# Kernel optimization log

Hardware: AMD Instinct MI355X
Metric: run time of the kernel (lower is better)

The kernel has to match this reference:

```python
import jax, jax.numpy as jnp
import numpy as np

HEADS = 4
NEG_SLOPE_ATT = 0.2   # GATConv default negative_slope
NEG_SLOPE_ACT = 0.01  # torch.nn.LeakyReLU default


def setup_inputs() -> dict:
    key = jax.random.key(0)
    ks = jax.random.split(key, 10)
    N, F_IN, C, NCLS, B = 100000, 128, 32, 10, 128
    E = 1600000
    x = jax.random.normal(ks[0], (N, F_IN), dtype=jnp.float32)
    edge_index = jax.random.randint(ks[1], (2, E), 0, N, dtype=jnp.int64)
    batch = jnp.sort(jax.random.randint(ks[2], (N,), 0, B, dtype=jnp.int64))
    # GATConv parameters (eval mode: dropout inactive)
    W = jax.random.normal(ks[3], (F_IN, HEADS * C), dtype=jnp.float32) / np.sqrt(F_IN)
    att_src = jax.random.normal(ks[4], (HEADS, C), dtype=jnp.float32) / np.sqrt(C)
    att_dst = jax.random.normal(ks[5], (HEADS, C), dtype=jnp.float32) / np.sqrt(C)
    bias = jnp.zeros((HEADS * C,), dtype=jnp.float32)
    lin_w = jax.random.normal(ks[6], (NCLS, HEADS * C), dtype=jnp.float32) / np.sqrt(HEADS * C)
    lin_b = jnp.zeros((NCLS,), dtype=jnp.float32)
    return {"x": x, "edge_index": edge_index, "batch": batch, "batch_size": B,
            "W": W, "att_src": att_src, "att_dst": att_dst, "bias": bias,
            "lin_w": lin_w, "lin_b": lin_b}


def _leaky(v, s):
    return jnp.where(v >= 0, v, s * v)


def reference(x, edge_index, batch, batch_size, W, att_src, att_dst, bias, lin_w, lin_b):
    N = x.shape[0]
    H, C = att_src.shape
    xh = (x @ W).reshape(N, H, C)                      # [N,H,C]
    # add self-loops (GATConv default add_self_loops=True)
    loops = jnp.arange(N, dtype=edge_index.dtype)
    src = jnp.concatenate([edge_index[0], loops])      # [E+N]
    dst = jnp.concatenate([edge_index[1], loops])
    a_src = jnp.einsum('nhc,hc->nh', xh, att_src)      # [N,H]
    a_dst = jnp.einsum('nhc,hc->nh', xh, att_dst)
    e = _leaky(a_src[src] + a_dst[dst], NEG_SLOPE_ATT) # [E+N,H]
    # segment softmax over incoming edges of each dst node
    m = jax.ops.segment_max(e, dst, num_segments=N)
    e = jnp.exp(e - m[dst])
    s = jax.ops.segment_sum(e, dst, num_segments=N)
    alpha = e / (s[dst] + 1e-16)                       # [E+N,H]
    msg = xh[src] * alpha[..., None]                   # [E+N,H,C]
    out = jax.ops.segment_sum(msg, dst, num_segments=N).reshape(N, H * C) + bias
    out = _leaky(out, NEG_SLOPE_ACT)
    # global mean pool per graph
    summed = jax.ops.segment_sum(out, batch, num_segments=batch_size)
    counts = jax.ops.segment_sum(jnp.ones((N,), dtype=out.dtype), batch, num_segments=batch_size)
    pooled = summed / jnp.maximum(counts, 1.0)[:, None]
    return pooled @ lin_w.T + lin_b
```

## Files before the change

kernel.cpp:

```cpp
#include <hip/hip_runtime.h>
#include <hip/hip_fp16.h>

#define HC 128
#define FIN 128
#define NHEAD 4
#define NS_ATT 0.2f
#define NS_ACT 0.01f
#define NBLK_P 256
#define BCAP 14336

typedef _Float16 half8 __attribute__((ext_vector_type(8)));
typedef float f32x4 __attribute__((ext_vector_type(4)));

__device__ __forceinline__ float lrelu(float v, float s) { return v >= 0.f ? v : s * v; }

__device__ __forceinline__ int lowerb(const int* __restrict__ a, int n, int v) {
  int lo = 0, hi = n;
  while (lo < hi) {
    int m = (lo + hi) >> 1;
    if (a[m] < v) lo = m + 1; else hi = m;
  }
  return lo;
}

__global__ __launch_bounds__(256) void k_hw(
    const int* __restrict__ ei, int* __restrict__ hist, int E, int NBUCK, int CH,
    const float* __restrict__ W, const float* __restrict__ att_s,
    const float* __restrict__ att_d, _Float16* __restrict__ Wh) {
  if (blockIdx.x >= NBLK_P) {
    const int nt = blockIdx.x - NBLK_P, t = threadIdx.x;
    const int kt = t >> 6, l = t & 63;
    const int c = nt * 16 + (l & 15);
    const int kbase = kt * 32 + (l >> 4) * 8;
    half8 v8;
#pragma unroll
    for (int j = 0; j < 8; ++j) {
      const int k = kbase + j;
      float v = 0.f;
      if (c < 128) {
        v = W[k * HC + c];
      } else if (c < 132) {
        const int h = c - 128;
        for (int cc = 0; cc < 32; ++cc) v += W[k * HC + h * 32 + cc] * att_s[h * 32 + cc];
      } else if (c < 136) {
        const int h = c - 132;
        for (int cc = 0; cc < 32; ++cc) v += W[k * HC + h * 32 + cc] * att_d[h * 32 + cc];
      }
      v8[j] = (_Float16)v;
    }
    ((half8*)Wh)[(nt * 4 + kt) * 64 + l] = v8;
    return;
  }
  __shared__ int lc[512];
  for (int i = threadIdx.x; i < NBUCK; i += 256) lc[i] = 0;
  __syncthreads();
  const int e0 = blockIdx.x * CH, e1 = min(E, e0 + CH);
  for (int e = e0 + threadIdx.x; e < e1; e += 256) {
    atomicAdd(&lc[ei[E + e] >> 9], 1);
  }
  __syncthreads();
  for (int i = threadIdx.x; i < NBUCK; i += 256) hist[i * NBLK_P + blockIdx.x] = lc[i];
}

__global__ __launch_bounds__(256) void k_xw(
    const float* __restrict__ x, const _Float16* __restrict__ Wh,
    _Float16* __restrict__ xh, float* __restrict__ a_src, float* __restrict__ a_dst,
    int N) {
  __shared__ _Float16 xs[4][16][HC + 8];
  const int wv = threadIdx.x >> 6, l = threadIdx.x & 63;
  const int r0 = blockIdx.x * 64 + wv * 16;
  if (r0 >= N) return;
  const int row_a = r0 + (l & 15);
  const long arow = (long)min(row_a, N - 1) * FIN;
  const int kg = (l >> 4) * 8;
  half8 afr[4];
#pragma unroll
  for (int kt = 0; kt < 4; ++kt) {
    const float4 p0 = *(const float4*)(x + arow + kt * 32 + kg);
    const float4 p1 = *(const float4*)(x + arow + kt * 32 + kg + 4);
    afr[kt][0] = (_Float16)p0.x; afr[kt][1] = (_Float16)p0.y;
    afr[kt][2] = (_Float16)p0.z; afr[kt][3] = (_Float16)p0.w;
    afr[kt][4] = (_Float16)p1.x; afr[kt][5] = (_Float16)p1.y;
    afr[kt][6] = (_Float16)p1.z; afr[kt][7] = (_Float16)p1.w;
  }
  const half8* __restrict__ Wh8 = (const half8*)Wh;
  const int rloc = (l >> 4) * 4;
  const int cc = l & 15;
#pragma unroll
  for (int nt = 0; nt < 9; ++nt) {
    half8 b0 = Wh8[(nt * 4 + 0) * 64 + l];
    half8 b1 = Wh8[(nt * 4 + 1) * 64 + l];
    half8 b2 = Wh8[(nt * 4 + 2) * 64 + l];
    half8 b3 = Wh8[(nt * 4 + 3) * 64 + l];
    f32x4 acc = {0.f, 0.f, 0.f, 0.f};
    acc = __builtin_amdgcn_mfma_f32_16x16x32_f16(afr[0], b0, acc, 0, 0, 0);
    acc = __builtin_amdgcn_mfma_f32_16x16x32_f16(afr[1], b1, acc, 0, 0, 0);
    acc = __builtin_amdgcn_mfma_f32_16x16x32_f16(afr[2], b2, acc, 0, 0, 0);
    acc = __builtin_amdgcn_mfma_f32_16x16x32_f16(afr[3], b3, acc, 0, 0, 0);
    if (nt < 8) {
      const int col = nt * 16 + cc;
#pragma unroll
      for (int r = 0; r < 4; ++r) xs[wv][rloc + r][col] = (_Float16)acc[r];
    } else if (cc < 8) {
      float* __restrict__ dst = (cc < 4) ? a_src : a_dst;
      const int h = cc & 3;
#pragma unroll
      for (int r = 0; r < 4; ++r) {
        const int row = r0 + rloc + r;
        if (row < N) dst[row * NHEAD + h] = acc[r];
      }
    }
  }
#pragma unroll
  for (int i = 0; i < 4; ++i) {
    const int lr = (l >> 4) + i * 4;
    const int row = r0 + lr;
    if (row < N) {
      const uint4 v = *(const uint4*)&xs[wv][lr][(l & 15) * 8];
      *(uint4*)(xh + (long)row * HC + (l & 15) * 8) = v;
    }
  }
}

__global__ void k_scanA(const int* __restrict__ cnt, int* __restrict__ offs,
                        int* __restrict__ part, int N) {
  __shared__ int s[256];
  int t = threadIdx.x, i = blockIdx.x * 256 + t;
  int v = (i < N) ? cnt[i] : 0;
  s[t] = v;
#pragma unroll
  for (int off = 1; off < 256; off <<= 1) {
    __syncthreads();
    int u = (t >= off) ? s[t - off] : 0;
    __syncthreads();
    s[t] += u;
  }
  if (i < N) offs[i] = s[t] - v;
  if (t == 255) part[blockIdx.x] = s[255];
}

__global__ void k_scanB(int* __restrict__ part, int NB) {
  __shared__ int s[1024];
  int t = threadIdx.x;
  int v = (t < NB) ? part[t] : 0;
  s[t] = v;
#pragma unroll
  for (int off = 1; off < 1024; off <<= 1) {
    __syncthreads();
    int u = (t >= off) ? s[t - off] : 0;
    __syncthreads();
    s[t] += u;
  }
  if (t < NB) part[t] = s[t] - v;
  if (t == 1023) part[NB] = s[1023];
}

__global__ void k_scanC(int* __restrict__ offs, const int* __restrict__ part, int N, int NB) {
  int i = blockIdx.x * 256 + threadIdx.x;
  if (i < N) offs[i] += part[i >> 8];
  else if (i == N) offs[N] = part[NB];
}

__global__ __launch_bounds__(256) void k_part(const int* __restrict__ ei,
                                              const int* __restrict__ histoffs,
                                              unsigned* __restrict__ ebuf,
                                              int E, int NBUCK, int CH) {
  __shared__ int lcur[512];
  for (int i = threadIdx.x; i < NBUCK; i += 256)
    lcur[i] = histoffs[i * NBLK_P + blockIdx.x];
  __syncthreads();
  const int e0 = blockIdx.x * CH, e1 = min(E, e0 + CH);
  for (int e = e0 + threadIdx.x; e < e1; e += 256) {
    const int s = ei[e], d = ei[E + e];
    const int pos = atomicAdd(&lcur[d >> 9], 1);
    ebuf[pos] = ((unsigned)(d & 511) << 18) | (unsigned)s;
  }
}

__global__ __launch_bounds__(256) void k_build(
    const int* __restrict__ histoffs, const unsigned* __restrict__ ebuf,
    int* __restrict__ csr_src, int* __restrict__ offs, int N) {
  const int b = blockIdx.x, t = threadIdx.x;
  const int n0 = b << 9, n1 = min(N, n0 + 512), nn = n1 - n0;
  const int eb0 = histoffs[b * NBLK_P];
  const int eb1 = histoffs[(b + 1) * NBLK_P];
  const int base = eb0 + n0;
  const int L = (eb1 - eb0) + nn;
  __shared__ int cnt2[512];
  __shared__ int scn[256];
  __shared__ int cur[512];
  __shared__ int lcsr[BCAP];
  cnt2[t] = 0; cnt2[t + 256] = 0;
  __syncthreads();
  for (int e = eb0 + t; e < eb1; e += 256) atomicAdd(&cnt2[ebuf[e] >> 18], 1);
  __syncthreads();
  const int i0 = 2 * t, i1 = 2 * t + 1;
  const int a0 = (i0 < nn) ? cnt2[i0] + 1 : 0;
  const int a1 = (i1 < nn) ? cnt2[i1] + 1 : 0;
  scn[t] = a0 + a1;
  for (int off = 1; off < 256; off <<= 1) {
    __syncthreads();
    int u = (t >= off) ? scn[t - off] : 0;
    __syncthreads();
    scn[t] += u;
  }
  __syncthreads();
  const int ex = scn[t] - (a0 + a1);
  const int o0 = ex, o1 = ex + a0;
  if (i0 < nn) offs[n0 + i0] = base + o0;
  if (i1 < nn) offs[n0 + i1] = base + o1;
  if (t == 255 && n1 == N) offs[N] = base + scn[255];
  if (L <= BCAP) {
    if (i0 < nn) { lcsr[o0] = n0 + i0; cur[i0] = o0 + 1; }
    if (i1 < nn) { lcsr[o1] = n0 + i1; cur[i1] = o1 + 1; }
    __syncthreads();
    for (int e = eb0 + t; e < eb1; e += 256) {
      const unsigned pk = ebuf[e];
      const int pos = atomicAdd(&cur[pk >> 18], 1);
      lcsr[pos] = (int)(pk & 0x3FFFFu);
    }
    __syncthreads();
    for (int i = t; i < L; i += 256) csr_src[base + i] = lcsr[i];
  } else {
    if (i0 < nn) { csr_src[base + o0] = n0 + i0; cur[i0] = base + o0 + 1; }
    if (i1 < nn) { csr_src[base + o1] = n0 + i1; cur[i1] = base + o1 + 1; }
    __syncthreads();
    for (int e = eb0 + t; e < eb1; e += 256) {
      const unsigned pk = ebuf[e];
      const int pos = atomicAdd(&cur[pk >> 18], 1);
      csr_src[pos] = (int)(pk & 0x3FFFFu);
    }
  }
}

__global__ __launch_bounds__(256) void k_agg(
    const int* __restrict__ csr_src, const int* __restrict__ offs,
    const float* __restrict__ a_src, const float* __restrict__ a_dst,
    const __half* __restrict__ xh, const float* __restrict__ bias,
    __half* __restrict__ xout, int N) {
  __shared__ float wls[4][64 * 5];
  __shared__ int sls[4][64];
  const int wv = threadIdx.x >> 6;
  const int wid = (blockIdx.x * 256 + threadIdx.x) >> 6;
  const int lane = threadIdx.x & 63;
  if (wid >= N) return;
  float* __restrict__ wl = wls[wv];
  int* __restrict__ sl = sls[wv];
  const int n = wid;
  const int o0 = offs[n], deg = offs[n + 1] - o0;
  const float4 dv = ((const float4*)a_dst)[n];
  const int l16 = lane & 15, g = lane >> 4, h = l16 >> 2;
  const uint4* __restrict__ xh16 = (const uint4*)xh;

  float4 sm = make_float4(0.f, 0.f, 0.f, 0.f);
  float acc[8] = {0.f, 0.f, 0.f, 0.f, 0.f, 0.f, 0.f, 0.f};

  for (int c0 = 0; c0 < deg; c0 += 64) {
    const int cl = min(64, deg - c0);
    if (lane < cl) {
      const int sj = csr_src[o0 + c0 + lane];
      const float4 av = ((const float4*)a_src)[sj];
      const float w0 = __expf(lrelu(av.x + dv.x, NS_ATT));
      const float w1 = __expf(lrelu(av.y + dv.y, NS_ATT));
      const float w2 = __expf(lrelu(av.z + dv.z, NS_ATT));
      const float w3 = __expf(lrelu(av.w + dv.w, NS_ATT));
      sm.x += w0; sm.y += w1; sm.z += w2; sm.w += w3;
      sl[lane] = sj;
      wl[lane * 5 + 0] = w0; wl[lane * 5 + 1] = w1;
      wl[lane * 5 + 2] = w2; wl[lane * 5 + 3] = w3;
    }
    for (int j = 0; j < cl; j += 16) {
      int s[4];
      float wsel[4];
      uint4 u[4];
#pragma unroll
      for (int q = 0; q < 4; ++q) {
        const int ee = j + q * 4 + g;
        const bool valid = ee < cl;
        const float wv_ = wl[ee * 5 + h];
        const int ss = sl[ee];
        wsel[q] = valid ? wv_ : 0.f;
        s[q] = valid ? ss : 0;
      }
#pragma unroll
      for (int q = 0; q < 4; ++q) {
        u[q] = xh16[(long)s[q] * 16 + l16];
      }
#pragma unroll
      for (int q = 0; q < 4; ++q) {
        const __half2* hp = (const __half2*)&u[q];
        const float2 f0 = __half22float2(hp[0]);
        const float2 f1 = __half22float2(hp[1]);
        const float2 f2 = __half22float2(hp[2]);
        const float2 f3 = __half22float2(hp[3]);
        acc[0] = fmaf(wsel[q], f0.x, acc[0]); acc[1] = fmaf(wsel[q], f0.y, acc[1]);
        acc[2] = fmaf(wsel[q], f1.x, acc[2]); acc[3] = fmaf(wsel[q], f1.y, acc[3]);
        acc[4] = fmaf(wsel[q], f2.x, acc[4]); acc[5] = fmaf(wsel[q], f2.y, acc[5]);
        acc[6] = fmaf(wsel[q], f3.x, acc[6]); acc[7] = fmaf(wsel[q], f3.y, acc[7]);
      }
    }
  }

#pragma unroll
  for (int m = 32; m >= 1; m >>= 1) {
    sm.x += __shfl_xor(sm.x, m);
    sm.y += __shfl_xor(sm.y, m);
    sm.z += __shfl_xor(sm.z, m);
    sm.w += __shfl_xor(sm.w, m);
  }
#pragma unroll
  for (int m = 32; m >= 16; m >>= 1) {
#pragma unroll
    for (int i = 0; i < 8; ++i) acc[i] += __shfl_xor(acc[i], m);
  }

  const float sh = (h == 0) ? sm.x : (h == 1) ? sm.y : (h == 2) ? sm.z : sm.w;
  const float inv = 1.f / (sh + 1e-16f);
  const int ch = l16 * 8 + g * 2;
  float r0 = lrelu(acc[2 * g] * inv + bias[ch], NS_ACT);
  float r1 = lrelu(acc[2 * g + 1] * inv + bias[ch + 1], NS_ACT);
  ((__half2*)(xout + (long)n * HC))[ch >> 1] = __floats2half2_rn(r0, r1);
}

__global__ __launch_bounds__(512) void k_poolfinal(
    const __half* __restrict__ xout, const int* __restrict__ batch,
    const float* __restrict__ lin_w, const float* __restrict__ lin_b,
    float* __restrict__ out, int N, int B) {
  const int b = blockIdx.x, t = threadIdx.x;
  const int lo = lowerb(batch, N, b);
  const int hi = lowerb(batch, N, b + 1);
  const int cnt = hi - lo;
  const int c2 = t & 63;
  const int rs = t >> 6;
  const __half2* __restrict__ xo2 = (const __half2*)xout;
  float ax = 0.f, ay = 0.f, bx2 = 0.f, by2 = 0.f;
  int r = lo + rs;
  for (; r + 8 < hi; r += 16) {
    float2 f0 = __half22float2(xo2[(long)r * 64 + c2]);
    float2 f1 = __half22float2(xo2[(long)(r + 8) * 64 + c2]);
    ax += f0.x; ay += f0.y; bx2 += f1.x; by2 += f1.y;
  }
  for (; r < hi; r += 8) {
    float2 f0 = __half22float2(xo2[(long)r * 64 + c2]);
    ax += f0.x; ay += f0.y;
  }
  __shared__ float2 sp[512];
  __shared__ float pl[HC];
  sp[t] = make_float2(ax + bx2, ay + by2);
  __syncthreads();
  if (t < 64) {
    float vx = 0.f, vy = 0.f;
#pragma unroll
    for (int i = 0; i < 8; ++i) {
      vx += sp[t + i * 64].x;
      vy += sp[t + i * 64].y;
    }
    const float c = fmaxf((float)cnt, 1.0f);
    pl[2 * t] = vx / c;
    pl[2 * t + 1] = vy / c;
  }
  __syncthreads();
  if (t < 10) {
    float a = lin_b[t];
    for (int k = 0; k < HC; ++k) a = fmaf(pl[k], lin_w[t * HC + k], a);
    out[b * 10 + t] = a;
  }
}

extern "C" void kernel_launch(void* const* d_in, const int* in_sizes, int n_in,
                              void* d_out, int out_size, void* d_ws, size_t ws_size,
                              hipStream_t stream) {
  const float* x = (const float*)d_in[0];
  const int* ei = (const int*)d_in[1];
  const int* batch = (const int*)d_in[2];
  const float* Wm = (const float*)d_in[4];
  const float* att_s = (const float*)d_in[5];
  const float* att_d = (const float*)d_in[6];
  const float* bias = (const float*)d_in[7];
  const float* lin_w = (const float*)d_in[8];
  const float* lin_b = (const float*)d_in[9];
  float* out = (float*)d_out;

  const int N = in_sizes[2];
  const int E = in_sizes[1] / 2;
  const int B = out_size / 10;
  const int NBUCK = (N + 511) >> 9;
  const int M = NBUCK * NBLK_P;
  const int NB2 = (M + 255) / 256;
  const int CH = (E + NBLK_P - 1) / NBLK_P;

  char* p = (char*)d_ws;
  auto carve = [&](size_t bytes) {
    void* r = (void*)p;
    p += (bytes + 255) & ~(size_t)255;
    return r;
  };
  __half* xh = (__half*)carve((size_t)N * HC * 2);
  __half* xout = (__half*)carve((size_t)N * HC * 2);
  float* a_src = (float*)carve((size_t)N * NHEAD * 4);
  float* a_dst = (float*)carve((size_t)N * NHEAD * 4);
  int* offs = (int*)carve((size_t)(N + 1) * 4);
  int* csr_src = (int*)carve((size_t)(N + (size_t)E) * 4);
  _Float16* Wh = (_Float16*)carve((size_t)9 * 4 * 64 * 8 * 2);

  char* q = (char*)xout;
  auto carve2 = [&](size_t bytes) {
    void* r = (void*)q;
    q += (bytes + 255) & ~(size_t)255;
    return r;
  };
  unsigned* ebuf = (unsigned*)carve2((size_t)E * 4);
  int* hist = (int*)carve2((size_t)M * 4);
  int* histoffs = (int*)carve2((size_t)(M + 1) * 4);
  int* part2 = (int*)carve2((size_t)(NB2 + 2) * 4);

  k_hw<<<NBLK_P + 9, 256, 0, stream>>>(ei, hist, E, NBUCK, CH, Wm, att_s, att_d, Wh);
  k_xw<<<(N + 63) / 64, 256, 0, stream>>>(x, Wh, (_Float16*)xh, a_src, a_dst, N);
  k_scanA<<<NB2, 256, 0, stream>>>(hist, histoffs, part2, M);
  k_scanB<<<1, 1024, 0, stream>>>(part2, NB2);
  k_scanC<<<(M + 256) / 256, 256, 0, stream>>>(histoffs, part2, M, NB2);
  k_part<<<NBLK_P, 256, 0, stream>>>(ei, histoffs, ebuf, E, NBUCK, CH);
  k_build<<<NBUCK, 256, 0, stream>>>(histoffs, ebuf, csr_src, offs, N);
  k_agg<<<(N + 3) / 4, 256, 0, stream>>>(csr_src, offs, a_src, a_dst, xh, bias, xout, N);
  k_poolfinal<<<B, 512, 0, stream>>>(xout, batch, lin_w, lin_b, out, N, B);
}
```

Baseline: 179.5 us.

## Fold histogram scan into partition kernel and merge histogram with XW GEMM

Removes the three separate scan kernels by having each partition block redundantly sum per-bucket counts across all 256 histogram blocks and scan the bucket totals itself. The edge histogram now runs as extra blocks of the x@W kernel instead of sharing a launch with weight prep, which gets its own small kernel. The aim is fewer kernel launches and serial dependencies. In exchange, every partition block does redundant global reads of the histogram, and the xs padding is enlarged.

```diff
diff --git a/kernel.cpp b/kernel.cpp
--- a/kernel.cpp
+++ b/kernel.cpp
@@ -23,50 +23,50 @@
   return lo;
 }
 
-__global__ __launch_bounds__(256) void k_hw(
-    const int* __restrict__ ei, int* __restrict__ hist, int E, int NBUCK, int CH,
-    const float* __restrict__ W, const float* __restrict__ att_s,
-    const float* __restrict__ att_d, _Float16* __restrict__ Wh) {
-  if (blockIdx.x >= NBLK_P) {
-    const int nt = blockIdx.x - NBLK_P, t = threadIdx.x;
-    const int kt = t >> 6, l = t & 63;
-    const int c = nt * 16 + (l & 15);
-    const int kbase = kt * 32 + (l >> 4) * 8;
-    half8 v8;
-#pragma unroll
-    for (int j = 0; j < 8; ++j) {
-      const int k = kbase + j;
-      float v = 0.f;
-      if (c < 128) {
-        v = W[k * HC + c];
-      } else if (c < 132) {
-        const int h = c - 128;
-        for (int cc = 0; cc < 32; ++cc) v += W[k * HC + h * 32 + cc] * att_s[h * 32 + cc];
-      } else if (c < 136) {
-        const int h = c - 132;
-        for (int cc = 0; cc < 32; ++cc) v += W[k * HC + h * 32 + cc] * att_d[h * 32 + cc];
-      }
-      v8[j] = (_Float16)v;
-    }
-    ((half8*)Wh)[(nt * 4 + kt) * 64 + l] = v8;
-    return;
-  }
-  __shared__ int lc[512];
-  for (int i = threadIdx.x; i < NBUCK; i += 256) lc[i] = 0;
-  __syncthreads();
-  const int e0 = blockIdx.x * CH, e1 = min(E, e0 + CH);
-  for (int e = e0 + threadIdx.x; e < e1; e += 256) {
-    atomicAdd(&lc[ei[E + e] >> 9], 1);
-  }
-  __syncthreads();
-  for (int i = threadIdx.x; i < NBUCK; i += 256) hist[i * NBLK_P + blockIdx.x] = lc[i];
-}
-
-__global__ __launch_bounds__(256) void k_xw(
+__global__ void k_wprep(const float* __restrict__ W, const float* __restrict__ att_s,
+                        const float* __restrict__ att_d, _Float16* __restrict__ Wh) {
+  const int nt = blockIdx.x, t = threadIdx.x;
+  const int kt = t >> 6, l = t & 63;
+  const int c = nt * 16 + (l & 15);
+  const int kbase = kt * 32 + (l >> 4) * 8;
+  half8 v8;
+#pragma unroll
+  for (int j = 0; j < 8; ++j) {
+    const int k = kbase + j;
+    float v = 0.f;
+    if (c < 128) {
+      v = W[k * HC + c];
+    } else if (c < 132) {
+      const int h = c - 128;
+      for (int cc = 0; cc < 32; ++cc) v += W[k * HC + h * 32 + cc] * att_s[h * 32 + cc];
+    } else if (c < 136) {
+      const int h = c - 132;
+      for (int cc = 0; cc < 32; ++cc) v += W[k * HC + h * 32 + cc] * att_d[h * 32 + cc];
+    }
+    v8[j] = (_Float16)v;
+  }
+  ((half8*)Wh)[(nt * 4 + kt) * 64 + l] = v8;
+}
+
+__global__ __launch_bounds__(256) void k_xwh(
     const float* __restrict__ x, const _Float16* __restrict__ Wh,
     _Float16* __restrict__ xh, float* __restrict__ a_src, float* __restrict__ a_dst,
-    int N) {
-  __shared__ _Float16 xs[4][16][HC + 8];
+    int N, int NXW,
+    const int* __restrict__ ei, int* __restrict__ hist, int E, int NBUCK, int CH) {
+  __shared__ _Float16 xs[4][16][HC + 16];
+  __shared__ int lc[512];
+  if (blockIdx.x >= NXW) {
+    const int b = blockIdx.x - NXW;
+    for (int i = threadIdx.x; i < NBUCK; i += 256) lc[i] = 0;
+    __syncthreads();
+    const int e0 = b * CH, e1 = min(E, e0 + CH);
+    for (int e = e0 + threadIdx.x; e < e1; e += 256) {
+      atomicAdd(&lc[ei[E + e] >> 9], 1);
+    }
+    __syncthreads();
+    for (int i = threadIdx.x; i < NBUCK; i += 256) hist[b * NBUCK + i] = lc[i];
+    return;
+  }
   const int wv = threadIdx.x >> 6, l = threadIdx.x & 63;
   const int r0 = blockIdx.x * 64 + wv * 16;
   if (r0 >= N) return;
@@ -122,55 +122,48 @@
   }
 }
 
-__global__ void k_scanA(const int* __restrict__ cnt, int* __restrict__ offs,
-                        int* __restrict__ part, int N) {
-  __shared__ int s[256];
-  int t = threadIdx.x, i = blockIdx.x * 256 + t;
-  int v = (i < N) ? cnt[i] : 0;
-  s[t] = v;
-#pragma unroll
-  for (int off = 1; off < 256; off <<= 1) {
-    __syncthreads();
-    int u = (t >= off) ? s[t - off] : 0;
-    __syncthreads();
-    s[t] += u;
-  }
-  if (i < N) offs[i] = s[t] - v;
-  if (t == 255) part[blockIdx.x] = s[255];
-}
-
-__global__ void k_scanB(int* __restrict__ part, int NB) {
-  __shared__ int s[1024];
-  int t = threadIdx.x;
-  int v = (t < NB) ? part[t] : 0;
-  s[t] = v;
-#pragma unroll
-  for (int off = 1; off < 1024; off <<= 1) {
-    __syncthreads();
-    int u = (t >= off) ? s[t - off] : 0;
-    __syncthreads();
-    s[t] += u;
-  }
-  if (t < NB) part[t] = s[t] - v;
-  if (t == 1023) part[NB] = s[1023];
-}
-
-__global__ void k_scanC(int* __restrict__ offs, const int* __restrict__ part, int N, int NB) {
-  int i = blockIdx.x * 256 + threadIdx.x;
-  if (i < N) offs[i] += part[i >> 8];
-  else if (i == N) offs[N] = part[NB];
-}
-
 __global__ __launch_bounds__(256) void k_part(const int* __restrict__ ei,
-                                              const int* __restrict__ histoffs,
+                                              const int* __restrict__ hist,
+                                              int* __restrict__ histbase,
                                               unsigned* __restrict__ ebuf,
                                               int E, int NBUCK, int CH) {
   __shared__ int lcur[512];
-  for (int i = threadIdx.x; i < NBUCK; i += 256)
-    lcur[i] = histoffs[i * NBLK_P + blockIdx.x];
-  __syncthreads();
-  const int e0 = blockIdx.x * CH, e1 = min(E, e0 + CH);
-  for (int e = e0 + threadIdx.x; e < e1; e += 256) {
+  __shared__ int tot[512];
+  __shared__ int scn[256];
+  const int b = blockIdx.x, t = threadIdx.x;
+  for (int i = t; i < NBUCK; i += 256) {
+    int sum = 0, pre = 0;
+    for (int bb = 0; bb < NBLK_P; ++bb) {
+      const int v = hist[bb * NBUCK + i];
+      sum += v;
+      if (bb < b) pre += v;
+    }
+    tot[i] = sum;
+    lcur[i] = pre;
+  }
+  __syncthreads();
+  const int i0 = 2 * t, i1 = 2 * t + 1;
+  const int a0 = (i0 < NBUCK) ? tot[i0] : 0;
+  const int a1 = (i1 < NBUCK) ? tot[i1] : 0;
+  scn[t] = a0 + a1;
+  for (int off = 1; off < 256; off <<= 1) {
+    __syncthreads();
+    int u = (t >= off) ? scn[t - off] : 0;
+    __syncthreads();
+    scn[t] += u;
+  }
+  __syncthreads();
+  const int ex = scn[t] - (a0 + a1);
+  if (i0 < NBUCK) lcur[i0] += ex;
+  if (i1 < NBUCK) lcur[i1] += ex + a0;
+  if (b == 0) {
+    if (i0 < NBUCK) histbase[i0] = ex;
+    if (i1 < NBUCK) histbase[i1] = ex + a0;
+    if (t == 255) histbase[NBUCK] = scn[255];
+  }
+  __syncthreads();
+  const int e0 = b * CH, e1 = min(E, e0 + CH);
+  for (int e = e0 + t; e < e1; e += 256) {
     const int s = ei[e], d = ei[E + e];
     const int pos = atomicAdd(&lcur[d >> 9], 1);
     ebuf[pos] = ((unsigned)(d & 511) << 18) | (unsigned)s;
@@ -178,12 +171,12 @@
 }
 
 __global__ __launch_bounds__(256) void k_build(
-    const int* __restrict__ histoffs, const unsigned* __restrict__ ebuf,
+    const int* __restrict__ histbase, const unsigned* __restrict__ ebuf,
     int* __restrict__ csr_src, int* __restrict__ offs, int N) {
   const int b = blockIdx.x, t = threadIdx.x;
   const int n0 = b << 9, n1 = min(N, n0 + 512), nn = n1 - n0;
-  const int eb0 = histoffs[b * NBLK_P];
-  const int eb1 = histoffs[(b + 1) * NBLK_P];
+  const int eb0 = histbase[b];
+  const int eb1 = histbase[b + 1];
   const int base = eb0 + n0;
   const int L = (eb1 - eb0) + nn;
   __shared__ int cnt2[512];
@@ -385,9 +378,8 @@
   const int E = in_sizes[1] / 2;
   const int B = out_size / 10;
   const int NBUCK = (N + 511) >> 9;
-  const int M = NBUCK * NBLK_P;
-  const int NB2 = (M + 255) / 256;
   const int CH = (E + NBLK_P - 1) / NBLK_P;
+  const int NXW = (N + 63) / 64;
 
   char* p = (char*)d_ws;
   auto carve = [&](size_t bytes) {
@@ -410,17 +402,14 @@
     return r;
   };
   unsigned* ebuf = (unsigned*)carve2((size_t)E * 4);
-  int* hist = (int*)carve2((size_t)M * 4);
-  int* histoffs = (int*)carve2((size_t)(M + 1) * 4);
-  int* part2 = (int*)carve2((size_t)(NB2 + 2) * 4);
-
-  k_hw<<<NBLK_P + 9, 256, 0, stream>>>(ei, hist, E, NBUCK, CH, Wm, att_s, att_d, Wh);
-  k_xw<<<(N + 63) / 64, 256, 0, stream>>>(x, Wh, (_Float16*)xh, a_src, a_dst, N);
-  k_scanA<<<NB2, 256, 0, stream>>>(hist, histoffs, part2, M);
-  k_scanB<<<1, 1024, 0, stream>>>(part2, NB2);
-  k_scanC<<<(M + 256) / 256, 256, 0, stream>>>(histoffs, part2, M, NB2);
-  k_part<<<NBLK_P, 256, 0, stream>>>(ei, histoffs, ebuf, E, NBUCK, CH);
-  k_build<<<NBUCK, 256, 0, stream>>>(histoffs, ebuf, csr_src, offs, N);
+  int* hist = (int*)carve2((size_t)NBLK_P * NBUCK * 4);
+  int* histbase = (int*)carve2((size_t)(NBUCK + 1) * 4);
+
+  k_wprep<<<9, 256, 0, stream>>>(Wm, att_s, att_d, Wh);
+  k_xwh<<<NXW + NBLK_P, 256, 0, stream>>>(x, Wh, (_Float16*)xh, a_src, a_dst, N, NXW,
+                                          ei, hist, E, NBUCK, CH);
+  k_part<<<NBLK_P, 256, 0, stream>>>(ei, hist, histbase, ebuf, E, NBUCK, CH);
+  k_build<<<NBUCK, 256, 0, stream>>>(histbase, ebuf, csr_src, offs, N);
   k_agg<<<(N + 3) / 4, 256, 0, stream>>>(csr_src, offs, a_src, a_dst, xh, bias, xout, N);
   k_poolfinal<<<B, 512, 0, stream>>>(xout, batch, lin_w, lin_b, out, N, B);
 }
```

Result: slower. 189.6 us (+5.6%).
